# Performance work log

Hardware: AMD Instinct MI355X
Metric: run time of the kernel (lower is better)

Reference implementation:

```python
import jax, jax.numpy as jnp
import numpy as np

VOCAB_SIZE = 8192
EMBED_DIM = 256


def setup_inputs() -> dict:
    key = jax.random.key(0)
    k1, k2 = jax.random.split(key)
    N = 16384  # batch(512) * num_slots(8) * tokens_per_slot(4)
    z = jax.random.normal(k1, (N, EMBED_DIM), dtype=jnp.float32)
    codebook = jax.random.normal(k2, (VOCAB_SIZE, EMBED_DIM), dtype=jnp.float32)
    return {"z": z, "codebook": codebook}


def reference(z, codebook):
    # Squared-distance cdist via the expansion ||z||^2 + ||e||^2 - 2 z.e^T
    z_sq = jnp.sum(z * z, axis=1, keepdims=True)            # [N, 1]
    e_sq = jnp.sum(codebook * codebook, axis=1)              # [V]
    dist = z_sq + e_sq - 2.0 * jnp.matmul(z, codebook.T)     # [N, V]
    tokens = jnp.argmin(dist, axis=-1)                       # [N] int
    z_q = codebook[tokens]                                   # [N, E] gather
    # one-hot reference count (side statistic in the original forward)
    ref_count = jnp.zeros((VOCAB_SIZE,), dtype=jnp.float32).at[tokens].add(1.0)
    return tokens, z_q, ref_count
```

## Files before the change

kernel.cpp:

```cpp
#include <hip/hip_runtime.h>
#include <math.h>

#define N_ROWS 16384
#define VOCAB  8192
#define EMB    256

#define BM 128
#define BV 128
#define BK 64
#define VSPLIT 8
#define VRANGE (VOCAB / VSPLIT)
#define NVT    (VRANGE / BV)
#define TAU 0.15f

typedef _Float16 half8 __attribute__((ext_vector_type(8)));
typedef _Float16 half4 __attribute__((ext_vector_type(4)));
typedef float floatx4 __attribute__((ext_vector_type(4)));

__device__ __forceinline__ void load_lds16(const _Float16* g, _Float16* l) {
    __builtin_amdgcn_global_load_lds(
        (const __attribute__((address_space(1))) void*)g,
        (__attribute__((address_space(3))) void*)l, 16, 0, 0);
}

__global__ void prep_kernel(const float* __restrict__ z, const float* __restrict__ cb,
                            _Float16* __restrict__ zh, _Float16* __restrict__ ch,
                            float* __restrict__ esq, float* __restrict__ cnt,
                            unsigned long long* __restrict__ rkey,
                            int* __restrict__ flagcnt) {
    const int b = blockIdx.x, t = threadIdx.x;
    if (b < VOCAB / 4) {
        const int row  = b * 4 + (t >> 6);
        const int lane = t & 63;
        const float4 f = *(const float4*)(cb + (size_t)row * EMB + lane * 4);
        half4 h;
        h.x = (_Float16)f.x; h.y = (_Float16)f.y; h.z = (_Float16)f.z; h.w = (_Float16)f.w;
        *(half4*)(ch + (size_t)row * EMB + lane * 4) = h;
        float s = f.x * f.x + f.y * f.y + f.z * f.z + f.w * f.w;
        #pragma unroll
        for (int off = 32; off > 0; off >>= 1) s += __shfl_down(s, off, 64);
        if (lane == 0) esq[row] = s;
        if (t < 4) cnt[b * 4 + t] = 0.0f;
        if (t >= 8 && t < 16) rkey[b * 8 + (t - 8)] = ~0ull;
        if (b == 0 && t == 4) flagcnt[0] = 0;
        if (b == 0 && t == 5) flagcnt[1] = 0;
    } else {
        const size_t idx4 = (size_t)(b - VOCAB / 4) * 256 + t;
        const float4 f = *(const float4*)(z + idx4 * 4);
        half4 h;
        h.x = (_Float16)f.x; h.y = (_Float16)f.y; h.z = (_Float16)f.z; h.w = (_Float16)f.w;
        *(half4*)(zh + idx4 * 4) = h;
    }
}

#define KSTEP(RD, WR, NKO, NCS, DOSTAGE)                                       \
    {                                                                          \
        __syncthreads();                                                       \
        if (DOSTAGE) {                                                         \
            const _Float16* ncs_ = (NCS);                                      \
            _Pragma("unroll")                                                  \
            for (int q = 0; q < 4; ++q) {                                      \
                load_lds16(zsrc + (size_t)q * 8 * EMB + (NKO),                 \
                           &zs[WR][w * 2048 + q * 512]);                       \
                load_lds16(ncs_ + (size_t)q * 8 * EMB + (NKO),                 \
                           &cs[WR][w * 2048 + q * 512]);                       \
            }                                                                  \
        }                                                                      \
        _Pragma("unroll")                                                      \
        for (int s_ = 0; s_ < 2; ++s_) {                                       \
            const int off_ = s_ ? offA1 : offA0;                               \
            half8 a_[4];                                                       \
            _Pragma("unroll")                                                  \
            for (int i_ = 0; i_ < 4; ++i_)                                     \
                a_[i_] = *(const half8*)&zs[RD][rA[i_] + off_];                \
            _Pragma("unroll")                                                  \
            for (int j_ = 0; j_ < 4; ++j_) {                                   \
                const half8 b_ = *(const half8*)&cs[RD][rB[j_] + off_];        \
                _Pragma("unroll")                                              \
                for (int i_ = 0; i_ < 4; ++i_)                                 \
                    acc[i_][j_] = __builtin_amdgcn_mfma_f32_16x16x32_f16(      \
                        a_[i_], b_, acc[i_][j_], 0, 0, 0);                     \
            }                                                                  \
        }                                                                      \
    }

__global__ __launch_bounds__(256, 2)
void mfma_dist_kernel(const _Float16* __restrict__ zh, const _Float16* __restrict__ ch,
                      const float* __restrict__ esq,
                      float* __restrict__ pd1, float* __restrict__ pd2,
                      float* __restrict__ pd3,
                      int* __restrict__ pi1, int* __restrict__ pi2) {
    __shared__ _Float16 zs[2][BM * BK];
    __shared__ _Float16 cs[2][BV * BK];
    float* sc_d1 = (float*)zs;
    float* sc_d2 = sc_d1 + BM * 2;
    float* sc_d3 = sc_d2 + BM * 2;
    int*   sc_i1 = (int*)(sc_d3 + BM * 2);
    int*   sc_i2 = sc_i1 + BM * 2;

    const int row0  = blockIdx.x * BM;
    const int vbase = blockIdx.y * VRANGE;

    const int tid  = threadIdx.x;
    const int w    = tid >> 6;
    const int lane = tid & 63;
    const int lr   = lane & 15;
    const int quad = lane >> 4;
    const int mh   = (w >> 1) * 64;
    const int vh   = (w & 1) * 64;

    const int q7   = quad ^ (lr & 7);
    const int offA0 = q7 * 8;
    const int offA1 = (4 ^ q7) * 8;
    int rA[4], rB[4];
    #pragma unroll
    for (int i = 0; i < 4; ++i) { rA[i] = (mh + i * 16 + lr) * BK; rB[i] = (vh + i * 16 + lr) * BK; }

    const int schunk = (lane & 7) ^ (lane >> 3);
    const _Float16* zsrc = zh + (size_t)(row0 + w * 32 + (lane >> 3)) * EMB + schunk * 8;

    float m1[16], m2[16], m3[16];
    #pragma unroll
    for (int t = 0; t < 16; ++t) { m1[t] = -INFINITY; m2[t] = -INFINITY; m3[t] = -INFINITY; }

    float ev[4];
    #pragma unroll
    for (int j = 0; j < 4; ++j) ev[j] = esq[vbase + vh + j * 16 + lr];

    {
        const _Float16* csrc0 = ch + (size_t)(vbase + w * 32 + (lane >> 3)) * EMB + schunk * 8;
        #pragma unroll
        for (int q = 0; q < 4; ++q) {
            load_lds16(zsrc  + (size_t)q * 8 * EMB, &zs[0][w * 2048 + q * 512]);
            load_lds16(csrc0 + (size_t)q * 8 * EMB, &cs[0][w * 2048 + q * 512]);
        }
    }

    for (int vt = 0; vt < NVT; ++vt) {
        const int v0 = vbase + vt * BV;
        const _Float16* csrc = ch + (size_t)(v0 + w * 32 + (lane >> 3)) * EMB + schunk * 8;

        floatx4 acc[4][4];
        #pragma unroll
        for (int j = 0; j < 4; ++j) {
            const float e2 = -0.5f * ev[j];
            #pragma unroll
            for (int i = 0; i < 4; ++i) acc[i][j] = (floatx4)e2;
        }
        float evn[4];
        {
            const int vtn = (vt + 1 < NVT) ? vt + 1 : vt;
            #pragma unroll
            for (int j = 0; j < 4; ++j) evn[j] = esq[vbase + vtn * BV + vh + j * 16 + lr];
        }

        KSTEP(0, 1, BK,     csrc, true)
        KSTEP(1, 0, 2 * BK, csrc, true)
        KSTEP(0, 1, 3 * BK, csrc, true)
        KSTEP(1, 0, 0,      csrc + (size_t)BV * EMB, (vt < NVT - 1))

        #pragma unroll
        for (int i = 0; i < 4; ++i) {
            #pragma unroll
            for (int reg = 0; reg < 4; ++reg) {
                const int t = i * 4 + reg;
                #pragma unroll
                for (int j = 0; j < 4; ++j) {
                    const unsigned code = ((unsigned)vt << 2) | (unsigned)j;
                    const float a = __uint_as_float(
                        (__float_as_uint(acc[i][j][reg]) & ~31u) | code);
                    const float mid = fminf(m1[t], a);
                    m1[t] = fmaxf(m1[t], a);
                    const float lo  = fminf(m2[t], mid);
                    m2[t] = fmaxf(m2[t], mid);
                    m3[t] = fmaxf(m3[t], lo);
                }
            }
        }
        #pragma unroll
        for (int j = 0; j < 4; ++j) ev[j] = evn[j];
    }

    int i1[16], i2[16];
    #pragma unroll
    for (int t = 0; t < 16; ++t) {
        const unsigned c1 = __float_as_uint(m1[t]) & 31u;
        const unsigned c2 = __float_as_uint(m2[t]) & 31u;
        i1[t] = vbase + (int)(c1 >> 2) * BV + vh + (int)(c1 & 3u) * 16 + lr;
        i2[t] = vbase + (int)(c2 >> 2) * BV + vh + (int)(c2 & 3u) * 16 + lr;
    }

    #pragma unroll
    for (int t = 0; t < 16; ++t) {
        float a1 = m1[t], a2 = m2[t], a3 = m3[t]; int ii1 = i1[t], ii2 = i2[t];
        #pragma unroll
        for (int off = 1; off < 16; off <<= 1) {
            const float o1 = __shfl_xor(a1, off, 64);
            const float o2 = __shfl_xor(a2, off, 64);
            const float o3 = __shfl_xor(a3, off, 64);
            const int  oi1 = __shfl_xor(ii1, off, 64);
            const int  oi2 = __shfl_xor(ii2, off, 64);
            const bool g1 = o1 > a1, g2 = o1 > a2, g3 = o1 > a3;
            a3  = g2 ? a2  : (g3 ? o1  : a3);
            a2  = g1 ? a1  : (g2 ? o1  : a2);
            ii2 = g1 ? ii1 : (g2 ? oi1 : ii2);
            a1  = g1 ? o1  : a1;
            ii1 = g1 ? oi1 : ii1;
            const bool h2 = o2 > a2, h3 = o2 > a3;
            a3  = h2 ? a2  : (h3 ? o2 : a3);
            a2  = h2 ? o2  : a2;
            ii2 = h2 ? oi2 : ii2;
            a3 = fmaxf(a3, o3);
        }
        m1[t] = a1; m2[t] = a2; m3[t] = a3; i1[t] = ii1; i2[t] = ii2;
    }
    if (lr == 0) {
        #pragma unroll
        for (int t = 0; t < 16; ++t) {
            const int r = mh + (t >> 2) * 16 + quad * 4 + (t & 3);
            sc_d1[r * 2 + (w & 1)] = m1[t];
            sc_d2[r * 2 + (w & 1)] = m2[t];
            sc_d3[r * 2 + (w & 1)] = m3[t];
            sc_i1[r * 2 + (w & 1)] = i1[t];
            sc_i2[r * 2 + (w & 1)] = i2[t];
        }
    }
    __syncthreads();
    if (tid < BM) {
        float a1 = sc_d1[tid * 2], a2 = sc_d2[tid * 2], a3 = sc_d3[tid * 2];
        int  ii1 = sc_i1[tid * 2], ii2 = sc_i2[tid * 2];
        const float o1 = sc_d1[tid * 2 + 1], o2 = sc_d2[tid * 2 + 1], o3 = sc_d3[tid * 2 + 1];
        const int  oi1 = sc_i1[tid * 2 + 1], oi2 = sc_i2[tid * 2 + 1];
        {
            const bool g1 = o1 > a1, g2 = o1 > a2, g3 = o1 > a3;
            a3  = g2 ? a2  : (g3 ? o1  : a3);
            a2  = g1 ? a1  : (g2 ? o1  : a2);
            ii2 = g1 ? ii1 : (g2 ? oi1 : ii2);
            a1  = g1 ? o1  : a1;
            ii1 = g1 ? oi1 : ii1;
            const bool h2 = o2 > a2, h3 = o2 > a3;
            a3  = h2 ? a2  : (h3 ? o2 : a3);
            a2  = h2 ? o2  : a2;
            ii2 = h2 ? oi2 : ii2;
            a3 = fmaxf(a3, o3);
        }
        const size_t o = (size_t)blockIdx.y * N_ROWS + row0 + tid;
        pd1[o] = -2.0f * a1; pd2[o] = -2.0f * a2; pd3[o] = -2.0f * a3;
        pi1[o] = ii1; pi2[o] = ii2;
    }
}
#undef KSTEP

__global__ void combine_kernel(const float* __restrict__ pd1, const float* __restrict__ pd2,
                               const float* __restrict__ pd3, const int* __restrict__ pi1,
                               const float* __restrict__ cb,
                               float* __restrict__ tokens, float* __restrict__ zq,
                               float* __restrict__ cnt,
                               int* __restrict__ flagcnt,
                               int* __restrict__ clist, int* __restrict__ flist) {
    const int wave = threadIdx.x >> 6;
    const int lane = threadIdx.x & 63;
    const int row  = blockIdx.x * 4 + wave;

    float g1 = INFINITY, g2 = INFINITY, mind3 = INFINITY; int gi = 0;
    #pragma unroll
    for (int s = 0; s < VSPLIT; ++s) {
        const size_t o = (size_t)s * N_ROWS + row;
        const float od1 = pd1[o], od2 = pd2[o], od3 = pd3[o]; const int oi1 = pi1[o];
        if (od1 < g1) { g2 = fminf(g1, od2); g1 = od1; gi = oi1; }
        else          { g2 = fminf(g2, od1); }
        mind3 = fminf(mind3, od3);
    }
    if ((g2 - g1) < TAU) {
        if (lane == 0) {
            if (mind3 >= g1 + TAU) {
                const int pos = atomicAdd(&flagcnt[0], 1);
                clist[pos] = row;
            } else {
                const int pos = atomicAdd(&flagcnt[1], 1);
                flist[pos] = row;
            }
        }
        return;
    }
    if (lane == 0) {
        tokens[row] = (float)gi;
        atomicAdd(&cnt[gi], 1.0f);
    }
    const float4 v = *(const float4*)(cb + (size_t)gi * EMB + lane * 4);
    *(float4*)(zq + (size_t)row * EMB + lane * 4) = v;
}

#define RBV 64
#define RSPLIT 4
#define NTILE (VOCAB / RBV)
#define CAND_BLOCKS 128
__global__ __launch_bounds__(256, 2)
void rescue_kernel(const int* __restrict__ flagcnt,
                   const int* __restrict__ clist, const int* __restrict__ flist,
                   const float* __restrict__ z, const float* __restrict__ cb,
                   const float* __restrict__ esq,
                   const int* __restrict__ pi1, const int* __restrict__ pi2,
                   float* __restrict__ tokens, float* __restrict__ zq,
                   float* __restrict__ cnt,
                   unsigned long long* __restrict__ rkey) {
    __shared__ float csf[RBV][EMB];

    const int tid  = threadIdx.x;
    const int w    = tid >> 6;
    const int lane = tid & 63;

    if (blockIdx.x < CAND_BLOCKS) {
        const int n = flagcnt[0];
        const int c = lane >> 2;
        const int s = lane & 3;

        for (int f = blockIdx.x * 4 + w; f < n; f += CAND_BLOCKS * 4) {
            const int row = clist[f];
            const size_t po = (size_t)(c & 7) * N_ROWS + row;
            const int cidx = (c < 8) ? pi1[po] : pi2[po];

            const float* zr = z  + (size_t)row  * EMB + s * 64;
            const float* cr = cb + (size_t)cidx * EMB + s * 64;
            float p0 = 0.0f, p1 = 0.0f, p2 = 0.0f, p3 = 0.0f;
            #pragma unroll
            for (int k = 0; k < 4; ++k) {
                const float4 z0 = *(const float4*)(zr + k * 16 + 0);
                const float4 c0 = *(const float4*)(cr + k * 16 + 0);
                const float4 z1 = *(const float4*)(zr + k * 16 + 4);
                const float4 c1 = *(const float4*)(cr + k * 16 + 4);
                const float4 z2 = *(const float4*)(zr + k * 16 + 8);
                const float4 c2 = *(const float4*)(cr + k * 16 + 8);
                const float4 z3 = *(const float4*)(zr + k * 16 + 12);
                const float4 c3 = *(const float4*)(cr + k * 16 + 12);
                p0 += z0.x * c0.x + z0.y * c0.y + z0.z * c0.z + z0.w * c0.w;
                p1 += z1.x * c1.x + z1.y * c1.y + z1.z * c1.z + z1.w * c1.w;
                p2 += z2.x * c2.x + z2.y * c2.y + z2.z * c2.z + z2.w * c2.w;
                p3 += z3.x * c3.x + z3.y * c3.y + z3.z * c3.z + z3.w * c3.w;
            }
            float p = (p0 + p1) + (p2 + p3);
            p += __shfl_xor(p, 1, 64);
            p += __shfl_xor(p, 2, 64);

            float bd = esq[cidx] - 2.0f * p;
            int   bv = cidx;
            #pragma unroll
            for (int off = 4; off < 64; off <<= 1) {
                const float od = __shfl_xor(bd, off, 64);
                const int   ov = __shfl_xor(bv, off, 64);
                if (od < bd || (od == bd && ov < bv)) { bd = od; bv = ov; }
            }
            if (lane == 0) {
                tokens[row] = (float)bv;
                atomicAdd(&cnt[bv], 1.0f);
            }
            const float4 c4 = *(const float4*)(cb + (size_t)bv * EMB + lane * 4);
            *(float4*)(zq + (size_t)row * EMB + lane * 4) = c4;
        }
        return;
    }

    const int n = __builtin_amdgcn_readfirstlane(flagcnt[1]);
    if (n == 0) return;

    const int bid  = blockIdx.x - CAND_BLOCKS;
    const int tile = bid >> 2;
    const int rs   = bid & 3;
    const int c0   = tile * RBV;
    const int g    = lane >> 2;
    const int s    = lane & 3;

    #pragma unroll
    for (int i = 0; i < 16; ++i) {
        const int code = i * 4 + w;
        const float4 v = *(const float4*)(cb + (size_t)(c0 + code) * EMB + lane * 4);
        *(float4*)&csf[code][(lane ^ (code & 7)) * 4] = v;
    }
    __syncthreads();

    const int nq = (n + 3) >> 2;
    const int q0 = (rs << 2) | w;
    if (q0 >= nq) return;

    float ev[4];
    #pragma unroll
    for (int gs = 0; gs < 4; ++gs) ev[gs] = esq[c0 + gs * 16 + g];

    for (int q = q0; q < nq; q += 16) {
        int rows[4];
        #pragma unroll
        for (int r = 0; r < 4; ++r) {
            const int fi = q * 4 + r;
            rows[r] = __builtin_amdgcn_readfirstlane(flist[fi < n ? fi : 0]);
        }

        float p[4][4];
        #pragma unroll
        for (int gs = 0; gs < 4; ++gs)
            #pragma unroll
            for (int r = 0; r < 4; ++r) p[gs][r] = 0.0f;

        #pragma unroll
        for (int kb = 0; kb < 4; ++kb) {
            #pragma unroll
            for (int kk = 0; kk < 4; ++kk) {
                const int dbase = (kb * 4 + kk) * 16 + s * 4;
                float4 zv[4];
                #pragma unroll
                for (int r = 0; r < 4; ++r)
                    zv[r] = *(const float4*)(z + (size_t)rows[r] * EMB + dbase);
                const int dq = (kb * 4 + kk) * 4 + s;
                #pragma unroll
                for (int gs = 0; gs < 4; ++gs) {
                    const int code = gs * 16 + g;
                    const float4 c4 = *(const float4*)&csf[code][(dq ^ (code & 7)) * 4];
                    #pragma unroll
                    for (int r = 0; r < 4; ++r)
                        p[gs][r] += zv[r].x * c4.x + zv[r].y * c4.y
                                  + zv[r].z * c4.z + zv[r].w * c4.w;
                }
            }
        }

        #pragma unroll
        for (int gs = 0; gs < 4; ++gs)
            #pragma unroll
            for (int r = 0; r < 4; ++r) {
                float t = p[gs][r];
                t += __shfl_xor(t, 1, 64);
                t += __shfl_xor(t, 2, 64);
                p[gs][r] = t;
            }

        #pragma unroll
        for (int r = 0; r < 4; ++r) {
            float bd = INFINITY; int bv = 0;
            #pragma unroll
            for (int gs = 0; gs < 4; ++gs) {
                const float d = ev[gs] - 2.0f * p[gs][r];
                const int v = c0 + gs * 16 + g;
                if (d < bd) { bd = d; bv = v; }
            }
            #pragma unroll
            for (int off = 4; off < 64; off <<= 1) {
                const float od = __shfl_xor(bd, off, 64);
                const int   ov = __shfl_xor(bv, off, 64);
                if (od < bd || (od == bd && ov < bv)) { bd = od; bv = ov; }
            }
            if (lane == 0 && q * 4 + r < n) {
                unsigned int u = __float_as_uint(bd);
                u = (u & 0x80000000u) ? ~u : (u | 0x80000000u);
                atomicMin(rkey + rows[r], ((unsigned long long)u << 32) | (unsigned int)bv);
            }
        }
    }
}

__global__ void rescue_write_kernel(const int* __restrict__ flagcnt,
                                    const int* __restrict__ flist,
                                    const unsigned long long* __restrict__ rkey,
                                    const float* __restrict__ cb,
                                    float* __restrict__ tokens, float* __restrict__ zq,
                                    float* __restrict__ cnt) {
    const int w    = threadIdx.x >> 6;
    const int lane = threadIdx.x & 63;
    const int n = flagcnt[1];
    for (int f = blockIdx.x * 4 + w; f < n; f += gridDim.x * 4) {
        const int row = flist[f];
        const int v = (int)(unsigned int)(rkey[row] & 0xFFFFFFFFull);
        if (lane == 0) {
            tokens[row] = (float)v;
            atomicAdd(&cnt[v], 1.0f);
        }
        const float4 c4 = *(const float4*)(cb + (size_t)v * EMB + lane * 4);
        *(float4*)(zq + (size_t)row * EMB + lane * 4) = c4;
    }
}

__global__ void esq_kernel(const float* __restrict__ cb, float* __restrict__ esq) {
    const int wave = threadIdx.x >> 6;
    const int lane = threadIdx.x & 63;
    const int row  = blockIdx.x * 4 + wave;
    const float4 v = *(const float4*)(cb + (size_t)row * EMB + lane * 4);
    float s = v.x * v.x + v.y * v.y + v.z * v.z + v.w * v.w;
    #pragma unroll
    for (int off = 32; off > 0; off >>= 1) s += __shfl_down(s, off, 64);
    if (lane == 0) esq[row] = s;
}

#define FLSTR 36
__global__ __launch_bounds__(256, 2)
void fb_dist_kernel(const float* __restrict__ z, const float* __restrict__ cb,
                    const float* __restrict__ esq,
                    float* __restrict__ pdist, int* __restrict__ pidx) {
    __shared__ float zs[BM][FLSTR];
    __shared__ float es[BV][FLSTR];
    __shared__ float rdist[16][16];
    __shared__ int   ridx [16][16];
    const int row0 = blockIdx.x * BM, vbase = blockIdx.y * VRANGE;
    const int tid = threadIdx.x, wave = tid >> 6, lane = tid & 63;
    const int wly = (lane >> 3) & 7, wlx = lane & 7;
    const int wbase = (wave >> 1) * 64, cbase = (wave & 1) * 64;
    const int arow = wbase + wly, bcol = cbase + wlx;
    const int rowSlot = (wave >> 1) * 8 + wly, colSlot = (wave & 1) * 8 + wlx;
    const int sc4 = tid & 7, sr0 = tid >> 3;
    float best[8]; int bidx[8];
    #pragma unroll
    for (int i = 0; i < 8; ++i) { best[i] = INFINITY; bidx[i] = 0; }
    for (int vt = 0; vt < NVT; ++vt) {
        const int v0 = vbase + vt * BV;
        float acc[8][8];
        #pragma unroll
        for (int i = 0; i < 8; ++i)
            #pragma unroll
            for (int j = 0; j < 8; ++j) acc[i][j] = 0.0f;
        #pragma unroll 1
        for (int kt = 0; kt < EMB / 32; ++kt) {
            #pragma unroll
            for (int t = 0; t < 4; ++t) {
                const int r = sr0 + 32 * t;
                *(float4*)&zs[r][sc4 * 4] = *(const float4*)(z  + (size_t)(row0 + r) * EMB + kt * 32 + sc4 * 4);
                *(float4*)&es[r][sc4 * 4] = *(const float4*)(cb + (size_t)(v0 + r) * EMB + kt * 32 + sc4 * 4);
            }
            __syncthreads();
            #pragma unroll 1
            for (int k0 = 0; k0 < 8; ++k0) {
                const int kk = k0 * 4;
                float a[8][4];
                #pragma unroll
                for (int i = 0; i < 8; ++i) {
                    const float4 a4 = *(const float4*)&zs[arow + 8 * i][kk];
                    a[i][0] = a4.x; a[i][1] = a4.y; a[i][2] = a4.z; a[i][3] = a4.w;
                }
                #pragma unroll
                for (int j = 0; j < 8; ++j) {
                    const float4 b4 = *(const float4*)&es[bcol + 8 * j][kk];
                    #pragma unroll
                    for (int i = 0; i < 8; ++i) {
                        acc[i][j] += a[i][0] * b4.x; acc[i][j] += a[i][1] * b4.y;
                        acc[i][j] += a[i][2] * b4.z; acc[i][j] += a[i][3] * b4.w;
                    }
                }
            }
            __syncthreads();
        }
        #pragma unroll
        for (int j = 0; j < 8; ++j) {
            const int v = v0 + bcol + 8 * j;
            const float evv = esq[v];
            #pragma unroll
            for (int i = 0; i < 8; ++i) {
                const float d = evv - 2.0f * acc[i][j];
                if (d < best[i]) { best[i] = d; bidx[i] = v; }
            }
        }
    }
    for (int i = 0; i < 8; ++i) {
        rdist[rowSlot][colSlot] = best[i];
        ridx [rowSlot][colSlot] = bidx[i];
        __syncthreads();
        if (colSlot == 0) {
            float bd = rdist[rowSlot][0]; int bi = ridx[rowSlot][0];
            #pragma unroll
            for (int t = 1; t < 16; ++t) {
                const float d = rdist[rowSlot][t]; const int ii = ridx[rowSlot][t];
                if (d < bd || (d == bd && ii < bi)) { bd = d; bi = ii; }
            }
            const int row = row0 + wbase + 8 * i + wly;
            pdist[(size_t)blockIdx.y * N_ROWS + row] = bd;
            pidx [(size_t)blockIdx.y * N_ROWS + row] = bi;
        }
        __syncthreads();
    }
}

__global__ void fb_combine_kernel(const float* __restrict__ pdist, const int* __restrict__ pidx,
                                  const float* __restrict__ cb,
                                  float* __restrict__ tokens, float* __restrict__ zq,
                                  float* __restrict__ cnt) {
    const int wave = threadIdx.x >> 6, lane = threadIdx.x & 63;
    const int row = blockIdx.x * 4 + wave;
    float bd = INFINITY; int bi = 0;
    #pragma unroll
    for (int s = 0; s < VSPLIT; ++s) {
        const float d = pdist[(size_t)s * N_ROWS + row];
        const int ii  = pidx [(size_t)s * N_ROWS + row];
        if (d < bd || (d == bd && ii < bi)) { bd = d; bi = ii; }
    }
    if (lane == 0) { tokens[row] = (float)bi; atomicAdd(&cnt[bi], 1.0f); }
    const float4 v = *(const float4*)(cb + (size_t)bi * EMB + lane * 4);
    *(float4*)(zq + (size_t)row * EMB + lane * 4) = v;
}

extern "C" void kernel_launch(void* const* d_in, const int* in_sizes, int n_in,
                              void* d_out, int out_size, void* d_ws, size_t ws_size,
                              hipStream_t stream) {
    const float* z  = (const float*)d_in[0];
    const float* cb = (const float*)d_in[1];

    float* out    = (float*)d_out;
    float* tokens = out;
    float* zq     = out + N_ROWS;
    float* cnt    = out + N_ROWS + (size_t)N_ROWS * EMB;

    const size_t ZE = (size_t)N_ROWS * EMB, CE = (size_t)VOCAB * EMB, P = (size_t)VSPLIT * N_ROWS;
    const size_t NEED = (ZE + CE) * sizeof(_Float16) + VOCAB * 4
                      + 5 * P * 4 + (size_t)N_ROWS * 8 + 256 + 2 * (size_t)N_ROWS * 4;

    if (ws_size >= NEED) {
        char* p = (char*)d_ws;
        _Float16* zh = (_Float16*)p;            p += ZE * 2;
        _Float16* ch = (_Float16*)p;            p += CE * 2;
        float* esq   = (float*)p;               p += VOCAB * 4;
        float* pd1   = (float*)p;               p += P * 4;
        float* pd2   = (float*)p;               p += P * 4;
        float* pd3   = (float*)p;               p += P * 4;
        int*   pi1   = (int*)p;                 p += P * 4;
        int*   pi2   = (int*)p;                 p += P * 4;
        unsigned long long* rkey = (unsigned long long*)p;  p += (size_t)N_ROWS * 8;
        int*   flagcnt = (int*)p;               p += 256;
        int*   clist = (int*)p;                 p += (size_t)N_ROWS * 4;
        int*   flist = (int*)p;

        prep_kernel<<<VOCAB / 4 + (int)(ZE / 4 / 256), 256, 0, stream>>>(
            z, cb, zh, ch, esq, cnt, rkey, flagcnt);
        mfma_dist_kernel<<<dim3(N_ROWS / BM, VSPLIT), 256, 0, stream>>>(
            zh, ch, esq, pd1, pd2, pd3, pi1, pi2);
        combine_kernel<<<N_ROWS / 4, 256, 0, stream>>>(
            pd1, pd2, pd3, pi1, cb, tokens, zq, cnt, flagcnt, clist, flist);
        rescue_kernel<<<CAND_BLOCKS + NTILE * RSPLIT, 256, 0, stream>>>(
            flagcnt, clist, flist, z, cb, esq, pi1, pi2, tokens, zq, cnt, rkey);
        rescue_write_kernel<<<32, 256, 0, stream>>>(
            flagcnt, flist, rkey, cb, tokens, zq, cnt);
    } else {
        float* esq   = (float*)d_ws;
        float* pdist = esq + VOCAB;
        int*   pidx  = (int*)(pdist + P);
        hipMemsetAsync(cnt, 0, VOCAB * sizeof(float), stream);
        esq_kernel<<<VOCAB / 4, 256, 0, stream>>>(cb, esq);
        fb_dist_kernel<<<dim3(N_ROWS / BM, VSPLIT), 256, 0, stream>>>(z, cb, esq, pdist, pidx);
        fb_combine_kernel<<<N_ROWS / 4, 256, 0, stream>>>(pdist, pidx, cb, tokens, zq, cnt);
    }
}
```

Baseline: 201.4 us.

## Widen vocab tile to two codebook blocks per iteration, drop LDS double buffering

Each iteration now computes two 128-wide codebook tiles (accA, accB) against the same z tile. Each z fragment loaded from LDS is reused across twice as many MFMAs, and the iteration count halves. The double-buffered LDS staging is replaced by single buffers with a sync before and after each K step, so loads for the next K slice no longer overlap the MFMAs on the current one. Accumulator register use doubles, which risks spills or lower occupancy under the two-blocks-per-CU launch bound.

Measured after the change: 294.6 us. 1.46x slower.

```diff
diff --git a/kernel.cpp b/kernel.cpp
--- a/kernel.cpp
+++ b/kernel.cpp
@@ -53,35 +53,45 @@
     }
 }
 
-#define KSTEP(RD, WR, NKO, NCS, DOSTAGE)                                       \
+#define KSTEP(KO, DOSTAGE)                                                     \
     {                                                                          \
-        __syncthreads();                                                       \
         if (DOSTAGE) {                                                         \
-            const _Float16* ncs_ = (NCS);                                      \
             _Pragma("unroll")                                                  \
             for (int q = 0; q < 4; ++q) {                                      \
-                load_lds16(zsrc + (size_t)q * 8 * EMB + (NKO),                 \
-                           &zs[WR][w * 2048 + q * 512]);                       \
-                load_lds16(ncs_ + (size_t)q * 8 * EMB + (NKO),                 \
-                           &cs[WR][w * 2048 + q * 512]);                       \
+                load_lds16(zsrc  + (size_t)q * 8 * EMB + (KO),                 \
+                           &zs [w * 2048 + q * 512]);                          \
+                load_lds16(csrcA + (size_t)q * 8 * EMB + (KO),                 \
+                           &csA[w * 2048 + q * 512]);                          \
+                load_lds16(csrcB + (size_t)q * 8 * EMB + (KO),                 \
+                           &csB[w * 2048 + q * 512]);                          \
             }                                                                  \
         }                                                                      \
+        __syncthreads();                                                       \
         _Pragma("unroll")                                                      \
         for (int s_ = 0; s_ < 2; ++s_) {                                       \
             const int off_ = s_ ? offA1 : offA0;                               \
             half8 a_[4];                                                       \
             _Pragma("unroll")                                                  \
             for (int i_ = 0; i_ < 4; ++i_)                                     \
-                a_[i_] = *(const half8*)&zs[RD][rA[i_] + off_];                \
+                a_[i_] = *(const half8*)&zs[rA[i_] + off_];                    \
             _Pragma("unroll")                                                  \
             for (int j_ = 0; j_ < 4; ++j_) {                                   \
-                const half8 b_ = *(const half8*)&cs[RD][rB[j_] + off_];        \
+                const half8 bA_ = *(const half8*)&csA[rB[j_] + off_];          \
                 _Pragma("unroll")                                              \
                 for (int i_ = 0; i_ < 4; ++i_)                                 \
-                    acc[i_][j_] = __builtin_amdgcn_mfma_f32_16x16x32_f16(      \
-                        a_[i_], b_, acc[i_][j_], 0, 0, 0);                     \
+                    accA[i_][j_] = __builtin_amdgcn_mfma_f32_16x16x32_f16(     \
+                        a_[i_], bA_, accA[i_][j_], 0, 0, 0);                   \
+            }                                                                  \
+            _Pragma("unroll")                                                  \
+            for (int j_ = 0; j_ < 4; ++j_) {                                   \
+                const half8 bB_ = *(const half8*)&csB[rB[j_] + off_];          \
+                _Pragma("unroll")                                              \
+                for (int i_ = 0; i_ < 4; ++i_)                                 \
+                    accB[i_][j_] = __builtin_amdgcn_mfma_f32_16x16x32_f16(     \
+                        a_[i_], bB_, accB[i_][j_], 0, 0, 0);                   \
             }                                                                  \
         }                                                                      \
+        __syncthreads();                                                       \
     }
 
 __global__ __launch_bounds__(256, 2)
@@ -90,8 +100,9 @@
                       float* __restrict__ pd1, float* __restrict__ pd2,
                       float* __restrict__ pd3,
                       int* __restrict__ pi1, int* __restrict__ pi2) {
-    __shared__ _Float16 zs[2][BM * BK];
-    __shared__ _Float16 cs[2][BV * BK];
+    __shared__ _Float16 zs[BM * BK];
+    __shared__ _Float16 csA[BV * BK];
+    __shared__ _Float16 csB[BV * BK];
     float* sc_d1 = (float*)zs;
     float* sc_d2 = sc_d1 + BM * 2;
     float* sc_d3 = sc_d2 + BM * 2;
@@ -123,41 +134,62 @@
     #pragma unroll
     for (int t = 0; t < 16; ++t) { m1[t] = -INFINITY; m2[t] = -INFINITY; m3[t] = -INFINITY; }
 
-    float ev[4];
-    #pragma unroll
-    for (int j = 0; j < 4; ++j) ev[j] = esq[vbase + vh + j * 16 + lr];
+    float evA[4], evB[4];
+    #pragma unroll
+    for (int j = 0; j < 4; ++j) {
+        evA[j] = esq[vbase + vh + j * 16 + lr];
+        evB[j] = esq[vbase + BV + vh + j * 16 + lr];
+    }
 
     {
-        const _Float16* csrc0 = ch + (size_t)(vbase + w * 32 + (lane >> 3)) * EMB + schunk * 8;
+        const _Float16* cA0 = ch + (size_t)(vbase + w * 32 + (lane >> 3)) * EMB + schunk * 8;
+        const _Float16* cB0 = cA0 + (size_t)BV * EMB;
         #pragma unroll
         for (int q = 0; q < 4; ++q) {
-            load_lds16(zsrc  + (size_t)q * 8 * EMB, &zs[0][w * 2048 + q * 512]);
-            load_lds16(csrc0 + (size_t)q * 8 * EMB, &cs[0][w * 2048 + q * 512]);
-        }
-    }
-
-    for (int vt = 0; vt < NVT; ++vt) {
-        const int v0 = vbase + vt * BV;
-        const _Float16* csrc = ch + (size_t)(v0 + w * 32 + (lane >> 3)) * EMB + schunk * 8;
-
-        floatx4 acc[4][4];
+            load_lds16(zsrc + (size_t)q * 8 * EMB, &zs [w * 2048 + q * 512]);
+            load_lds16(cA0  + (size_t)q * 8 * EMB, &csA[w * 2048 + q * 512]);
+            load_lds16(cB0  + (size_t)q * 8 * EMB, &csB[w * 2048 + q * 512]);
+        }
+    }
+
+    for (int it = 0; it < NVT / 2; ++it) {
+        const int vA = vbase + it * 2 * BV;
+        const _Float16* csrcA = ch + (size_t)(vA + w * 32 + (lane >> 3)) * EMB + schunk * 8;
+        const _Float16* csrcB = csrcA + (size_t)BV * EMB;
+
+        floatx4 accA[4][4], accB[4][4];
         #pragma unroll
         for (int j = 0; j < 4; ++j) {
-            const float e2 = -0.5f * ev[j];
-            #pragma unroll
-            for (int i = 0; i < 4; ++i) acc[i][j] = (floatx4)e2;
-        }
-        float evn[4];
+            const float eA = -0.5f * evA[j];
+            const float eB = -0.5f * evB[j];
+            #pragma unroll
+            for (int i = 0; i < 4; ++i) { accA[i][j] = (floatx4)eA; accB[i][j] = (floatx4)eB; }
+        }
+        float evnA[4], evnB[4];
         {
-            const int vtn = (vt + 1 < NVT) ? vt + 1 : vt;
-            #pragma unroll
-            for (int j = 0; j < 4; ++j) evn[j] = esq[vbase + vtn * BV + vh + j * 16 + lr];
-        }
-
-        KSTEP(0, 1, BK,     csrc, true)
-        KSTEP(1, 0, 2 * BK, csrc, true)
-        KSTEP(0, 1, 3 * BK, csrc, true)
-        KSTEP(1, 0, 0,      csrc + (size_t)BV * EMB, (vt < NVT - 1))
+            const int itn = (it + 1 < NVT / 2) ? it + 1 : it;
+            #pragma unroll
+            for (int j = 0; j < 4; ++j) {
+                evnA[j] = esq[vbase + itn * 2 * BV + vh + j * 16 + lr];
+                evnB[j] = esq[vbase + itn * 2 * BV + BV + vh + j * 16 + lr];
+            }
+        }
+
+        KSTEP(0,      false)
+        KSTEP(BK,     true)
+        KSTEP(2 * BK, true)
+        KSTEP(3 * BK, true)
+
+        if (it + 1 < NVT / 2) {
+            const _Float16* nA = csrcA + (size_t)2 * BV * EMB;
+            const _Float16* nB = nA + (size_t)BV * EMB;
+            #pragma unroll
+            for (int q = 0; q < 4; ++q) {
+                load_lds16(zsrc + (size_t)q * 8 * EMB, &zs [w * 2048 + q * 512]);
+                load_lds16(nA   + (size_t)q * 8 * EMB, &csA[w * 2048 + q * 512]);
+                load_lds16(nB   + (size_t)q * 8 * EMB, &csB[w * 2048 + q * 512]);
+            }
+        }
 
         #pragma unroll
         for (int i = 0; i < 4; ++i) {
@@ -166,19 +198,30 @@
                 const int t = i * 4 + reg;
                 #pragma unroll
                 for (int j = 0; j < 4; ++j) {
-                    const unsigned code = ((unsigned)vt << 2) | (unsigned)j;
+                    const unsigned code = ((unsigned)it << 3) | (unsigned)j;
                     const float a = __uint_as_float(
-                        (__float_as_uint(acc[i][j][reg]) & ~31u) | code);
+                        (__float_as_uint(accA[i][j][reg]) & ~31u) | code);
                     const float mid = fminf(m1[t], a);
                     m1[t] = fmaxf(m1[t], a);
                     const float lo  = fminf(m2[t], mid);
                     m2[t] = fmaxf(m2[t], mid);
                     m3[t] = fmaxf(m3[t], lo);
                 }
-            }
-        }
-        #pragma unroll
-        for (int j = 0; j < 4; ++j) ev[j] = evn[j];
+                #pragma unroll
+                for (int j = 0; j < 4; ++j) {
+                    const unsigned code = ((unsigned)it << 3) | 4u | (unsigned)j;
+                    const float a = __uint_as_float(
+                        (__float_as_uint(accB[i][j][reg]) & ~31u) | code);
+                    const float mid = fminf(m1[t], a);
+                    m1[t] = fmaxf(m1[t], a);
+                    const float lo  = fminf(m2[t], mid);
+                    m2[t] = fmaxf(m2[t], mid);
+                    m3[t] = fmaxf(m3[t], lo);
+                }
+            }
+        }
+        #pragma unroll
+        for (int j = 0; j < 4; ++j) { evA[j] = evnA[j]; evB[j] = evnB[j]; }
     }
 
     int i1[16], i2[16];
```
